# Kernel tuning notes

Measured on AMD Instinct MI355X. Metric: run time of the kernel, lower is better.

The kernel has to match this reference:

```python
import jax, jax.numpy as jnp
import numpy as np
import math

NUM_HEADS = 12
SPARSITY = 0.2


def setup_inputs() -> dict:
    key = jax.random.key(0)
    ks = jax.random.split(key, 4)
    B, N, C = 8, 1024, 768
    x = jax.random.normal(ks[0], (B, N, C), dtype=jnp.float32)
    origin = jax.random.normal(ks[1], (B, N, C), dtype=jnp.float32)
    W_qkv = jax.random.normal(ks[2], (C, 3 * C), dtype=jnp.float32) * (C ** -0.5)
    W_proj = jax.random.normal(ks[3], (C, C), dtype=jnp.float32) * (C ** -0.5)
    b_proj = jnp.zeros((C,), dtype=jnp.float32)
    return {"x": x, "origin": origin, "W_qkv": W_qkv, "W_proj": W_proj, "b_proj": b_proj}


def reference(x, origin, W_qkv, W_proj, b_proj):
    B, N, C = x.shape
    H = NUM_HEADS
    hd = C // H
    scale = hd ** -0.5
    # qkv projection (no bias), split into q,k,v of shape [B,H,N,hd]
    qkv = (x @ W_qkv).reshape(B, N, 3, H, hd).transpose(2, 0, 3, 1, 4)
    q, k, v = qkv[0], qkv[1], qkv[2]
    # scaled scores with constant bias log(1 + N/197); bias is constant so softmax unaffected,
    # but keep it for faithfulness (threshold is taken on post-softmax values anyway)
    logits = jnp.einsum('bhqd,bhkd->bhqk', q * scale, k) + math.log(1.0 + N / 197.0)
    attn = jax.nn.softmax(logits, axis=-1)  # [B,H,N,N]
    # global per-batch threshold: keep top sparsity fraction of all H*N*N scores
    total = H * N * N
    k_idx = int(total * SPARSITY) - 1  # index in descending order
    attn_flat = attn.reshape(B, total)
    thr = jnp.sort(attn_flat, axis=-1)[:, total - 1 - k_idx]  # ascending sort, pick k-th largest
    attn = jnp.where(attn >= thr[:, None, None, None], attn, jnp.zeros((), attn.dtype))
    # attention output, merge heads, project, residual
    out = jnp.einsum('bhqk,bhkd->bhqd', attn, v).transpose(0, 2, 1, 3).reshape(B, N, C)
    out = out @ W_proj + b_proj
    return out + origin
```

## Files before the change

### kernel.cpp

```cpp
#include <hip/hip_runtime.h>
#include <hip/hip_bf16.h>

#define BATCH 8
#define SEQ   1024
#define CDIM  768
#define HEADS 12
#define HD    64

#define NB1    2048
#define TMIN2  (-24.0f)
#define W2     (24.0f / (float)NB1)
#define INV_W2 ((float)NB1 / 24.0f)
#define HLSTR  (NB1 + 8)
#define K_SUB  314573u
#define QSCALE 0.18033688011112042f

typedef __attribute__((ext_vector_type(8)))  short bf16x8;
typedef __attribute__((ext_vector_type(4)))  short bf16x4;
typedef __attribute__((ext_vector_type(4)))  float f32x4;
typedef __attribute__((ext_vector_type(16))) float f32x16;
typedef __attribute__((ext_vector_type(4)))  unsigned u32x4;
typedef __attribute__((ext_vector_type(2)))  unsigned u32x2;

#define MFMA16(a, b, c) __builtin_amdgcn_mfma_f32_16x16x32_bf16(a, b, c, 0, 0, 0)
#define MFMA32(a, b, c) __builtin_amdgcn_mfma_f32_32x32x16_bf16(a, b, c, 0, 0, 0)
#define EXP2(x) __builtin_amdgcn_exp2f(x)
#define LOG2(x) __builtin_amdgcn_logf(x)

__device__ inline unsigned cvtpk(float lo, float hi) {
    unsigned r;
    asm("v_cvt_pk_bf16_f32 %0, %1, %2" : "=v"(r) : "v"(lo), "v"(hi));
    return r;
}

__global__ __launch_bounds__(256) void prep_all(const float* __restrict__ x,
                                                const float* __restrict__ Wq,
                                                const float* __restrict__ Wp,
                                                short* __restrict__ xb,
                                                short* __restrict__ wqt,
                                                short* __restrict__ wpt) {
    __shared__ float ls[64][68];
    int bid = blockIdx.x, tid = threadIdx.x;
    if (bid < 3072) {
        int i = bid * 256 + tid;
        float4 a = *reinterpret_cast<const float4*>(&x[(size_t)i * 8]);
        float4 b = *reinterpret_cast<const float4*>(&x[(size_t)i * 8 + 4]);
        u32x4 w = {cvtpk(a.x, a.y), cvtpk(a.z, a.w), cvtpk(b.x, b.y), cvtpk(b.z, b.w)};
        *reinterpret_cast<u32x4*>(&xb[(size_t)i * 8]) = w;
        return;
    }
    const float* in;
    short* out;
    int C, t;
    if (bid < 3504) { t = bid - 3072; in = Wq; out = wqt; C = 2304; }
    else            { t = bid - 3504; in = Wp; out = wpt; C = 768; }
    int r0 = (t % 12) * 64, c0 = (t / 12) * 64;
#pragma unroll
    for (int it = 0; it < 4; ++it) {
        int rr = it * 16 + (tid >> 4);
        int cc = (tid & 15) * 4;
        float4 d = *reinterpret_cast<const float4*>(&in[(size_t)(r0 + rr) * C + c0 + cc]);
        ls[rr][cc + 0] = d.x; ls[rr][cc + 1] = d.y; ls[rr][cc + 2] = d.z; ls[rr][cc + 3] = d.w;
    }
    __syncthreads();
#pragma unroll
    for (int it = 0; it < 2; ++it) {
        int orow = it * 32 + (tid >> 3);
        int oc = (tid & 7) * 8;
        u32x4 w = {cvtpk(ls[oc + 0][orow], ls[oc + 1][orow]),
                   cvtpk(ls[oc + 2][orow], ls[oc + 3][orow]),
                   cvtpk(ls[oc + 4][orow], ls[oc + 5][orow]),
                   cvtpk(ls[oc + 6][orow], ls[oc + 7][orow])};
        *reinterpret_cast<u32x4*>(&out[(size_t)(c0 + orow) * 768 + r0 + oc]) = w;
    }
}

__global__ __launch_bounds__(256) void qkv_mfma(const short* __restrict__ A,
                                                const short* __restrict__ Bt,
                                                __hip_bfloat16* __restrict__ q,
                                                __hip_bfloat16* __restrict__ k,
                                                __hip_bfloat16* __restrict__ vt) {
    const int K = 768;
    __shared__ short As[128 * 64];
    __shared__ short Bs[128 * 64];
    int tM = blockIdx.x * 128, tN = blockIdx.y * 128;
    int tid = threadIdx.x, wave = tid >> 6, lane = tid & 63, lg = lane >> 4, lc = lane & 15;
    int wr = wave >> 1, wc = wave & 1;
    int srow = tid >> 3, scol = (tid & 7) * 8;
    f32x4 acc[4][4] = {};

    bf16x8 sa[4], sb[4];
#pragma unroll
    for (int j = 0; j < 4; ++j) {
        int r = j * 32 + srow;
        sa[j] = *(const bf16x8*)&A[(size_t)(tM + r) * K + scol];
        sb[j] = *(const bf16x8*)&Bt[(size_t)(tN + r) * K + scol];
    }
#pragma unroll
    for (int j = 0; j < 4; ++j) {
        int r = j * 32 + srow;
        int sw = scol ^ ((r & 7) << 3);
        *(bf16x8*)&As[r * 64 + sw] = sa[j];
        *(bf16x8*)&Bs[r * 64 + sw] = sb[j];
    }
    __syncthreads();

    for (int kc = 0; kc < K; kc += 64) {
        if (kc + 64 < K) {
#pragma unroll
            for (int j = 0; j < 4; ++j) {
                int r = j * 32 + srow;
                sa[j] = *(const bf16x8*)&A[(size_t)(tM + r) * K + kc + 64 + scol];
                sb[j] = *(const bf16x8*)&Bt[(size_t)(tN + r) * K + kc + 64 + scol];
            }
        }
        bf16x8 af[4][2], bfr[4][2];
#pragma unroll
        for (int m4 = 0; m4 < 4; ++m4) {
            int r = wr * 64 + m4 * 16 + lc;
            int sw = (r & 7) << 3;
            af[m4][0] = *(bf16x8*)&As[r * 64 + ((lg * 8) ^ sw)];
            af[m4][1] = *(bf16x8*)&As[r * 64 + ((32 + lg * 8) ^ sw)];
        }
#pragma unroll
        for (int n4 = 0; n4 < 4; ++n4) {
            int r = wc * 64 + n4 * 16 + lc;
            int sw = (r & 7) << 3;
            bfr[n4][0] = *(bf16x8*)&Bs[r * 64 + ((lg * 8) ^ sw)];
            bfr[n4][1] = *(bf16x8*)&Bs[r * 64 + ((32 + lg * 8) ^ sw)];
        }
#pragma unroll
        for (int m4 = 0; m4 < 4; ++m4)
#pragma unroll
            for (int n4 = 0; n4 < 4; ++n4) {
                acc[m4][n4] = MFMA16(af[m4][0], bfr[n4][0], acc[m4][n4]);
                acc[m4][n4] = MFMA16(af[m4][1], bfr[n4][1], acc[m4][n4]);
            }
        __syncthreads();
        if (kc + 64 < K) {
#pragma unroll
            for (int j = 0; j < 4; ++j) {
                int r = j * 32 + srow;
                int sw = scol ^ ((r & 7) << 3);
                *(bf16x8*)&As[r * 64 + sw] = sa[j];
                *(bf16x8*)&Bs[r * 64 + sw] = sb[j];
            }
            __syncthreads();
        }
    }
    int three = tN / 768;
    int cbase = tN - three * 768 + wc * 64;
    if (three == 2) {
#pragma unroll
        for (int m4 = 0; m4 < 4; ++m4) {
            int row0 = tM + wr * 64 + m4 * 16 + lg * 4;
            int b = row0 >> 10, n0 = row0 & 1023;
#pragma unroll
            for (int n4 = 0; n4 < 4; ++n4) {
                int cw = cbase + n4 * 16 + lc;
                int h = cw >> 6, d = cw & 63;
                u32x2 w = {cvtpk(acc[m4][n4][0], acc[m4][n4][1]),
                           cvtpk(acc[m4][n4][2], acc[m4][n4][3])};
                *reinterpret_cast<u32x2*>(
                    &vt[(((size_t)(b * HEADS + h) * 64 + d) << 10) + n0]) = w;
            }
        }
    } else {
        __hip_bfloat16* dst = (three == 0) ? q : k;
#pragma unroll
        for (int m4 = 0; m4 < 4; ++m4)
#pragma unroll
            for (int n4 = 0; n4 < 4; ++n4) {
                int cw = cbase + n4 * 16 + lc;
                int h = cw >> 6, d = cw & 63;
#pragma unroll
                for (int r = 0; r < 4; r += 2) {
                    int row = tM + wr * 64 + m4 * 16 + lg * 4 + r;
                    int b = row >> 10, n = row & 1023;
                    float v0 = acc[m4][n4][r], v1 = acc[m4][n4][r + 1];
                    if (three == 0) { v0 *= QSCALE; v1 *= QSCALE; }
                    unsigned w = cvtpk(v0, v1);
                    size_t base = (((size_t)(b * HEADS + h) << 10) + n) * HD + d;
                    *(unsigned short*)&dst[base] = (unsigned short)w;
                    *(unsigned short*)&dst[base + HD] = (unsigned short)(w >> 16);
                }
            }
    }
}

__global__ __launch_bounds__(256) void stats_mfma(const short* __restrict__ q,
                                                  const short* __restrict__ k,
                                                  float* __restrict__ orow,
                                                  unsigned* __restrict__ hist) {
    __shared__ short kls[8192];
    __shared__ unsigned hl[2 * HLSTR];
    int bid = (blockIdx.x & 7) * 96 + (blockIdx.x >> 3);
    int grp = bid & 7;
    int bh = bid >> 3;
    int b = bh / HEADS;
    int tid = threadIdx.x, wave = tid >> 6, lane = tid & 63;
    int ql = lane & 31, h = lane >> 5;
    const short* kbase = k + (size_t)bh * SEQ * HD;
    int qrow0 = grp * 128 + wave * 32;
    const short* qbase = q + ((size_t)bh * SEQ + qrow0) * HD;
    bf16x8 qf[4];
#pragma unroll
    for (int f = 0; f < 4; ++f)
        qf[f] = *(const bf16x8*)&qbase[ql * 64 + f * 16 + h * 8];

    for (int i = tid; i < 2 * HLSTR; i += 256) hl[i] = 0;

    int srow = tid >> 3, scol = (tid & 7) * 8;
    unsigned scache[4][8];

    bf16x8 st[4];
#pragma unroll
    for (int j = 0; j < 4; ++j)
        st[j] = *(const bf16x8*)&kbase[(size_t)(j * 32 + srow) * 64 + scol];
#pragma unroll
    for (int j = 0; j < 4; ++j) {
        int r = j * 32 + srow;
        *(bf16x8*)&kls[r * 64 + (scol ^ ((r & 7) << 3))] = st[j];
    }
    __syncthreads();
    float lsum = 0.f;
#pragma unroll
    for (int c = 0; c < 8; ++c) {
        if (c < 7) {
#pragma unroll
            for (int j = 0; j < 4; ++j)
                st[j] = *(const bf16x8*)&kbase[(size_t)((c + 1) * 128 + j * 32 + srow) * 64 + scol];
        }
#pragma unroll
        for (int kT = 0; kT < 4; ++kT) {
            f32x16 acc = {};
#pragma unroll
            for (int f = 0; f < 4; ++f) {
                int krow = kT * 32 + ql;
                bf16x8 af = *(bf16x8*)&kls[krow * 64 + ((f * 16 + h * 8) ^ ((krow & 7) << 3))];
                acc = MFMA32(af, qf[f], acc);
            }
            if (kT == 0 && (c & 1) == 0) {
#pragma unroll
                for (int i = 0; i < 8; ++i)
                    scache[c >> 1][i] = cvtpk(acc[2 * i], acc[2 * i + 1]);
            }
            float s = 0.f;
#pragma unroll
            for (int r = 0; r < 16; ++r) s += EXP2(acc[r]);
            lsum += s;
        }
        __syncthreads();
        if (c < 7) {
#pragma unroll
            for (int j = 0; j < 4; ++j) {
                int r = j * 32 + srow;
                *(bf16x8*)&kls[r * 64 + (scol ^ ((r & 7) << 3))] = st[j];
            }
            __syncthreads();
        }
    }
    lsum += __shfl_xor(lsum, 32, 64);
    float o = LOG2(lsum);
    if (h == 0) orow[(size_t)bh * SEQ + qrow0 + ql] = o;

    unsigned coff = (lane & 1) * HLSTR;
#pragma unroll
    for (int cc = 0; cc < 4; ++cc)
#pragma unroll
        for (int i = 0; i < 8; ++i) {
            unsigned w = scache[cc][i];
            float s0 = __builtin_bit_cast(float, w << 16);
            float s1 = __builtin_bit_cast(float, w & 0xffff0000u);
            int b0 = (int)((s0 - o) * INV_W2 + (float)NB1);
            int b1 = (int)((s1 - o) * INV_W2 + (float)NB1);
            b0 = b0 < 0 ? 0 : (b0 > NB1 - 1 ? NB1 - 1 : b0);
            b1 = b1 < 0 ? 0 : (b1 > NB1 - 1 ? NB1 - 1 : b1);
            atomicAdd(&hl[coff + b0], 1u);
            atomicAdd(&hl[coff + b1], 1u);
        }
    __syncthreads();
    unsigned* hb = hist + (size_t)b * NB1;
    for (int i = tid; i < NB1; i += 256) {
        unsigned s = hl[i] + hl[HLSTR + i];
        if (s) atomicAdd(&hb[i], s);
    }
}

__global__ __launch_bounds__(256) void find_thr(const unsigned* __restrict__ hist,
                                                float* __restrict__ thr) {
    __shared__ unsigned cs[256];
    int b = blockIdx.x, tid = threadIdx.x;
    const unsigned* hb = hist + (size_t)b * NB1;
    unsigned s = 0;
#pragma unroll
    for (int i = 0; i < 8; ++i) s += hb[tid * 8 + i];
    cs[tid] = s;
    __syncthreads();
    unsigned suf = 0;
    for (int j = tid; j < 256; ++j) suf += cs[j];
    unsigned above = suf - cs[tid];
    if (suf >= K_SUB && above < K_SUB) {
        unsigned acc = above;
        for (int bb = 7; bb >= 0; --bb) {
            acc += hb[tid * 8 + bb];
            if (acc >= K_SUB) {
                thr[b] = TMIN2 + (float)(tid * 8 + bb) * W2;
                break;
            }
        }
    }
}

__global__ __launch_bounds__(256) void pv_mfma(const short* __restrict__ q,
                                               const short* __restrict__ k,
                                               const short* __restrict__ vt,
                                               const float* __restrict__ orow,
                                               const float* __restrict__ thr,
                                               __hip_bfloat16* __restrict__ aout) {
    __shared__ __align__(16) char smem[32768];
    short* klsA = (short*)smem;
    short* klsB = (short*)(smem + 8192);
    short* vlsA = (short*)(smem + 16384);
    short* vlsB = (short*)(smem + 24576);
    float* comb = (float*)smem;

    int bid = (blockIdx.x & 7) * 192 + (blockIdx.x >> 3);
    int grp = bid & 15;
    int bh = bid >> 4;
    int b = bh / HEADS, hh = bh % HEADS;
    int tid = threadIdx.x, wave = tid >> 6, lane = tid & 63;
    int ql = lane & 31, h = lane >> 5;
    int rh = wave & 1;
    int kh = wave >> 1;
    const short* kbase = k + (size_t)bh * SEQ * HD;
    const short* vtb = vt + (size_t)bh * HD * SEQ;
    int qrow0 = grp * 64 + rh * 32;
    const short* qbase = q + ((size_t)bh * SEQ + qrow0) * HD;
    bf16x8 qf[4];
#pragma unroll
    for (int f = 0; f < 4; ++f)
        qf[f] = *(const bf16x8*)&qbase[ql * 64 + f * 16 + h * 8];
    float o = orow[(size_t)bh * SEQ + qrow0 + ql];
    float tt = thr[b];
    f32x16 oacc[2] = {};
    f32x16 minus_o;
#pragma unroll
    for (int r = 0; r < 16; ++r) minus_o[r] = -o;

    short* kls = kh ? klsB : klsA;
    short* vls = kh ? vlsB : vlsA;

    int sp = tid >> 7;
    int tl = tid & 127;
    int srow = tl >> 3, scol = (tl & 7) * 8;
    short* skls = sp ? klsB : klsA;
    short* svls = sp ? vlsB : vlsA;

    bf16x8 sk[4], sv[4];
    int cc0 = sp * 8;
#pragma unroll
    for (int j = 0; j < 4; ++j) {
        int r = j * 16 + srow;
        sk[j] = *(const bf16x8*)&kbase[(size_t)(cc0 * 64 + r) * 64 + scol];
        sv[j] = *(const bf16x8*)&vtb[((size_t)r << 10) + cc0 * 64 + scol];
    }
#pragma unroll
    for (int j = 0; j < 4; ++j) {
        int r = j * 16 + srow;
        *(bf16x8*)&skls[r * 64 + (scol ^ ((r & 7) << 3))] = sk[j];
        *(bf16x8*)&svls[r * 64 + (scol ^ ((r & 7) << 3))] = sv[j];
    }
    __syncthreads();

    for (int c = 0; c < 8; ++c) {
        if (c < 7) {
            int cc = sp * 8 + c + 1;
#pragma unroll
            for (int j = 0; j < 4; ++j) {
                int r = j * 16 + srow;
                sk[j] = *(const bf16x8*)&kbase[(size_t)(cc * 64 + r) * 64 + scol];
                sv[j] = *(const bf16x8*)&vtb[((size_t)r << 10) + cc * 64 + scol];
            }
        }
#pragma unroll
        for (int kT = 0; kT < 2; ++kT) {
            f32x16 acc = minus_o;
#pragma unroll
            for (int f = 0; f < 4; ++f) {
                int krow = kT * 32 + ql;
                bf16x8 af = *(bf16x8*)&kls[krow * 64 + ((f * 16 + h * 8) ^ ((krow & 7) << 3))];
                acc = MFMA32(af, qf[f], acc);
            }
            float p[16];
#pragma unroll
            for (int r = 0; r < 16; ++r)
                p[r] = (acc[r] >= tt) ? EXP2(acc[r]) : 0.f;
            unsigned c8[8];
#pragma unroll
            for (int i = 0; i < 8; ++i) c8[i] = cvtpk(p[2 * i], p[2 * i + 1]);
#pragma unroll
            for (int s = 0; s < 2; ++s) {
                unsigned a1 = c8[4 * s],     b1 = c8[4 * s + 2];
                unsigned a2 = c8[4 * s + 1], b2 = c8[4 * s + 3];
                asm("v_permlane32_swap_b32 %0, %1" : "+v"(a1), "+v"(b1));
                asm("v_permlane32_swap_b32 %0, %1" : "+v"(a2), "+v"(b2));
                u32x4 W = {a1, a2, b1, b2};
                bf16x8 pa = __builtin_bit_cast(bf16x8, W);
#pragma unroll
                for (int dt = 0; dt < 2; ++dt) {
                    int vrow = dt * 32 + ql;
                    int vcol = (kT * 32 + s * 16 + h * 8) ^ ((vrow & 7) << 3);
                    bf16x8 vf = *(bf16x8*)&vls[vrow * 64 + vcol];
                    oacc[dt] = MFMA32(pa, vf, oacc[dt]);
                }
            }
        }
        __syncthreads();
        if (c < 7) {
#pragma unroll
            for (int j = 0; j < 4; ++j) {
                int r = j * 16 + srow;
                *(bf16x8*)&skls[r * 64 + (scol ^ ((r & 7) << 3))] = sk[j];
                *(bf16x8*)&svls[r * 64 + (scol ^ ((r & 7) << 3))] = sv[j];
            }
            __syncthreads();
        }
    }

    if (kh == 1) {
#pragma unroll
        for (int dt = 0; dt < 2; ++dt)
#pragma unroll
            for (int r = 0; r < 16; ++r) {
                int crow = (r & 3) + 8 * (r >> 2) + 4 * h;
                comb[(rh * 32 + crow) * 65 + dt * 32 + ql] = oacc[dt][r];
            }
    }
    __syncthreads();
    if (kh == 1) return;
#pragma unroll
    for (int dt = 0; dt < 2; ++dt)
#pragma unroll
        for (int r = 0; r < 16; ++r) {
            int crow = (r & 3) + 8 * (r >> 2) + 4 * h;
            oacc[dt][r] += comb[(rh * 32 + crow) * 65 + dt * 32 + ql];
        }
#pragma unroll
    for (int dt = 0; dt < 2; ++dt)
#pragma unroll
        for (int r = 0; r < 16; r += 2) {
            int qr0 = qrow0 + (r & 3) + 8 * (r >> 2) + 4 * h;
            int qr1 = qrow0 + ((r + 1) & 3) + 8 * ((r + 1) >> 2) + 4 * h;
            unsigned w = cvtpk(oacc[dt][r], oacc[dt][r + 1]);
            *(unsigned short*)&aout[((size_t)b * SEQ + qr0) * CDIM + hh * 64 + dt * 32 + ql] =
                (unsigned short)w;
            *(unsigned short*)&aout[((size_t)b * SEQ + qr1) * CDIM + hh * 64 + dt * 32 + ql] =
                (unsigned short)(w >> 16);
        }
}

__global__ __launch_bounds__(256) void proj_mfma(const short* __restrict__ A,
                                                 const short* __restrict__ Bt,
                                                 const float* __restrict__ bias,
                                                 const float* __restrict__ origin,
                                                 float* __restrict__ out) {
    const int K = 768, NN = 768;
    __shared__ short As[128 * 64];
    __shared__ short Bs[128 * 64];
    int tM = blockIdx.x * 128, tN = blockIdx.y * 128;
    int tid = threadIdx.x, wave = tid >> 6, lane = tid & 63, lg = lane >> 4, lc = lane & 15;
    int wr = wave >> 1, wc = wave & 1;
    int srow = tid >> 3, scol = (tid & 7) * 8;
    f32x4 acc[4][4] = {};

    bf16x8 sa[4], sb[4];
#pragma unroll
    for (int j = 0; j < 4; ++j) {
        int r = j * 32 + srow;
        sa[j] = *(const bf16x8*)&A[(size_t)(tM + r) * K + scol];
        sb[j] = *(const bf16x8*)&Bt[(size_t)(tN + r) * K + scol];
    }
#pragma unroll
    for (int j = 0; j < 4; ++j) {
        int r = j * 32 + srow;
        int sw = scol ^ ((r & 7) << 3);
        *(bf16x8*)&As[r * 64 + sw] = sa[j];
        *(bf16x8*)&Bs[r * 64 + sw] = sb[j];
    }
    __syncthreads();

    for (int kc = 0; kc < K; kc += 64) {
        if (kc + 64 < K) {
#pragma unroll
            for (int j = 0; j < 4; ++j) {
                int r = j * 32 + srow;
                sa[j] = *(const bf16x8*)&A[(size_t)(tM + r) * K + kc + 64 + scol];
                sb[j] = *(const bf16x8*)&Bt[(size_t)(tN + r) * K + kc + 64 + scol];
            }
        }
        bf16x8 af[4][2], bfr[4][2];
#pragma unroll
        for (int m4 = 0; m4 < 4; ++m4) {
            int r = wr * 64 + m4 * 16 + lc;
            int sw = (r & 7) << 3;
            af[m4][0] = *(bf16x8*)&As[r * 64 + ((lg * 8) ^ sw)];
            af[m4][1] = *(bf16x8*)&As[r * 64 + ((32 + lg * 8) ^ sw)];
        }
#pragma unroll
        for (int n4 = 0; n4 < 4; ++n4) {
            int r = wc * 64 + n4 * 16 + lc;
            int sw = (r & 7) << 3;
            bfr[n4][0] = *(bf16x8*)&Bs[r * 64 + ((lg * 8) ^ sw)];
            bfr[n4][1] = *(bf16x8*)&Bs[r * 64 + ((32 + lg * 8) ^ sw)];
        }
#pragma unroll
        for (int m4 = 0; m4 < 4; ++m4)
#pragma unroll
            for (int n4 = 0; n4 < 4; ++n4) {
                acc[m4][n4] = MFMA16(af[m4][0], bfr[n4][0], acc[m4][n4]);
                acc[m4][n4] = MFMA16(af[m4][1], bfr[n4][1], acc[m4][n4]);
            }
        __syncthreads();
        if (kc + 64 < K) {
#pragma unroll
            for (int j = 0; j < 4; ++j) {
                int r = j * 32 + srow;
                int sw = scol ^ ((r & 7) << 3);
                *(bf16x8*)&As[r * 64 + sw] = sa[j];
                *(bf16x8*)&Bs[r * 64 + sw] = sb[j];
            }
            __syncthreads();
        }
    }
#pragma unroll
    for (int m4 = 0; m4 < 4; ++m4)
#pragma unroll
        for (int n4 = 0; n4 < 4; ++n4)
#pragma unroll
            for (int r = 0; r < 4; ++r) {
                int row = tM + wr * 64 + m4 * 16 + lg * 4 + r;
                int col = tN + wc * 64 + n4 * 16 + lc;
                out[(size_t)row * NN + col] = acc[m4][n4][r] + bias[col] + origin[(size_t)row * NN + col];
            }
}

extern "C" void kernel_launch(void* const* d_in, const int* in_sizes, int n_in,
                              void* d_out, int out_size, void* d_ws, size_t ws_size,
                              hipStream_t stream) {
    const float* x      = (const float*)d_in[0];
    const float* origin = (const float*)d_in[1];
    const float* W_qkv  = (const float*)d_in[2];
    const float* W_proj = (const float*)d_in[3];
    const float* b_proj = (const float*)d_in[4];
    float* out = (float*)d_out;
    char* ws = (char*)d_ws;

    const size_t QKV_ELEMS = (size_t)BATCH * HEADS * SEQ * HD;
    const size_t X_ELEMS   = (size_t)BATCH * SEQ * CDIM;
    size_t off = 0;
    short* xb  = (short*)(ws + off); off += X_ELEMS * 2;
    short* wqt = (short*)(ws + off); off += (size_t)2304 * 768 * 2;
    short* wpt = (short*)(ws + off); off += (size_t)768 * 768 * 2;
    short* q   = (short*)(ws + off); off += QKV_ELEMS * 2;
    short* k   = (short*)(ws + off); off += QKV_ELEMS * 2;
    short* vt  = (short*)(ws + off); off += QKV_ELEMS * 2;
    short* aoutb = (short*)(ws + off); off += QKV_ELEMS * 2;
    float* orow = (float*)(ws + off); off += (size_t)BATCH * HEADS * SEQ * 4;
    unsigned* hist = (unsigned*)(ws + off); off += (size_t)BATCH * NB1 * 4;
    float* thr = (float*)(ws + off); off += 8 * 4;

    hipMemsetAsync(hist, 0, (size_t)BATCH * NB1 * sizeof(unsigned), stream);
    prep_all<<<dim3(3648), 256, 0, stream>>>(x, W_qkv, W_proj, xb, wqt, wpt);
    qkv_mfma<<<dim3(64, 18), 256, 0, stream>>>(xb, wqt,
                                               (__hip_bfloat16*)q, (__hip_bfloat16*)k, (__hip_bfloat16*)vt);
    stats_mfma<<<dim3(BATCH * HEADS * 8), 256, 0, stream>>>(q, k, orow, hist);
    find_thr<<<dim3(BATCH), 256, 0, stream>>>(hist, thr);
    pv_mfma<<<dim3(BATCH * HEADS * 16), 256, 0, stream>>>(q, k, vt, orow, thr,
                                                          (__hip_bfloat16*)aoutb);
    proj_mfma<<<dim3(64, 6), 256, 0, stream>>>(aoutb, wpt, b_proj, origin, out);
}
```

Before: 158.9 us.

## Fuse x bf16 conversion into QKV GEMM loads and histogram zeroing into prep

```diff
diff --git a/kernel.cpp b/kernel.cpp
--- a/kernel.cpp
+++ b/kernel.cpp
@@ -33,27 +33,19 @@
     return r;
 }
 
-__global__ __launch_bounds__(256) void prep_all(const float* __restrict__ x,
-                                                const float* __restrict__ Wq,
+__global__ __launch_bounds__(256) void prep_all(const float* __restrict__ Wq,
                                                 const float* __restrict__ Wp,
-                                                short* __restrict__ xb,
                                                 short* __restrict__ wqt,
-                                                short* __restrict__ wpt) {
+                                                short* __restrict__ wpt,
+                                                unsigned* __restrict__ hist) {
     __shared__ float ls[64][68];
     int bid = blockIdx.x, tid = threadIdx.x;
-    if (bid < 3072) {
-        int i = bid * 256 + tid;
-        float4 a = *reinterpret_cast<const float4*>(&x[(size_t)i * 8]);
-        float4 b = *reinterpret_cast<const float4*>(&x[(size_t)i * 8 + 4]);
-        u32x4 w = {cvtpk(a.x, a.y), cvtpk(a.z, a.w), cvtpk(b.x, b.y), cvtpk(b.z, b.w)};
-        *reinterpret_cast<u32x4*>(&xb[(size_t)i * 8]) = w;
-        return;
-    }
+    if (bid < 64) hist[bid * 256 + tid] = 0u;
     const float* in;
     short* out;
     int C, t;
-    if (bid < 3504) { t = bid - 3072; in = Wq; out = wqt; C = 2304; }
-    else            { t = bid - 3504; in = Wp; out = wpt; C = 768; }
+    if (bid < 432) { t = bid; in = Wq; out = wqt; C = 2304; }
+    else           { t = bid - 432; in = Wp; out = wpt; C = 768; }
     int r0 = (t % 12) * 64, c0 = (t / 12) * 64;
 #pragma unroll
     for (int it = 0; it < 4; ++it) {
@@ -75,7 +67,7 @@
     }
 }
 
-__global__ __launch_bounds__(256) void qkv_mfma(const short* __restrict__ A,
+__global__ __launch_bounds__(256) void qkv_mfma(const float* __restrict__ X,
                                                 const short* __restrict__ Bt,
                                                 __hip_bfloat16* __restrict__ q,
                                                 __hip_bfloat16* __restrict__ k,
@@ -89,18 +81,21 @@
     int srow = tid >> 3, scol = (tid & 7) * 8;
     f32x4 acc[4][4] = {};
 
-    bf16x8 sa[4], sb[4];
+    u32x4 sa[4];
+    bf16x8 sb[4];
 #pragma unroll
     for (int j = 0; j < 4; ++j) {
         int r = j * 32 + srow;
-        sa[j] = *(const bf16x8*)&A[(size_t)(tM + r) * K + scol];
+        float4 xa = *reinterpret_cast<const float4*>(&X[(size_t)(tM + r) * K + scol]);
+        float4 xb2 = *reinterpret_cast<const float4*>(&X[(size_t)(tM + r) * K + scol + 4]);
+        sa[j] = u32x4{cvtpk(xa.x, xa.y), cvtpk(xa.z, xa.w), cvtpk(xb2.x, xb2.y), cvtpk(xb2.z, xb2.w)};
         sb[j] = *(const bf16x8*)&Bt[(size_t)(tN + r) * K + scol];
     }
 #pragma unroll
     for (int j = 0; j < 4; ++j) {
         int r = j * 32 + srow;
         int sw = scol ^ ((r & 7) << 3);
-        *(bf16x8*)&As[r * 64 + sw] = sa[j];
+        *(u32x4*)&As[r * 64 + sw] = sa[j];
         *(bf16x8*)&Bs[r * 64 + sw] = sb[j];
     }
     __syncthreads();
@@ -110,7 +105,9 @@
 #pragma unroll
             for (int j = 0; j < 4; ++j) {
                 int r = j * 32 + srow;
-                sa[j] = *(const bf16x8*)&A[(size_t)(tM + r) * K + kc + 64 + scol];
+                float4 xa = *reinterpret_cast<const float4*>(&X[(size_t)(tM + r) * K + kc + 64 + scol]);
+                float4 xb2 = *reinterpret_cast<const float4*>(&X[(size_t)(tM + r) * K + kc + 64 + scol + 4]);
+                sa[j] = u32x4{cvtpk(xa.x, xa.y), cvtpk(xa.z, xa.w), cvtpk(xb2.x, xb2.y), cvtpk(xb2.z, xb2.w)};
                 sb[j] = *(const bf16x8*)&Bt[(size_t)(tN + r) * K + kc + 64 + scol];
             }
         }
@@ -142,7 +139,7 @@
             for (int j = 0; j < 4; ++j) {
                 int r = j * 32 + srow;
                 int sw = scol ^ ((r & 7) << 3);
-                *(bf16x8*)&As[r * 64 + sw] = sa[j];
+                *(u32x4*)&As[r * 64 + sw] = sa[j];
                 *(bf16x8*)&Bs[r * 64 + sw] = sb[j];
             }
             __syncthreads();
@@ -557,9 +554,7 @@
     char* ws = (char*)d_ws;
 
     const size_t QKV_ELEMS = (size_t)BATCH * HEADS * SEQ * HD;
-    const size_t X_ELEMS   = (size_t)BATCH * SEQ * CDIM;
     size_t off = 0;
-    short* xb  = (short*)(ws + off); off += X_ELEMS * 2;
     short* wqt = (short*)(ws + off); off += (size_t)2304 * 768 * 2;
     short* wpt = (short*)(ws + off); off += (size_t)768 * 768 * 2;
     short* q   = (short*)(ws + off); off += QKV_ELEMS * 2;
@@ -570,9 +565,8 @@
     unsigned* hist = (unsigned*)(ws + off); off += (size_t)BATCH * NB1 * 4;
     float* thr = (float*)(ws + off); off += 8 * 4;
 
-    hipMemsetAsync(hist, 0, (size_t)BATCH * NB1 * sizeof(unsigned), stream);
-    prep_all<<<dim3(3648), 256, 0, stream>>>(x, W_qkv, W_proj, xb, wqt, wpt);
-    qkv_mfma<<<dim3(64, 18), 256, 0, stream>>>(xb, wqt,
+    prep_all<<<dim3(576), 256, 0, stream>>>(W_qkv, W_proj, wqt, wpt, hist);
+    qkv_mfma<<<dim3(64, 18), 256, 0, stream>>>(x, wqt,
                                                (__hip_bfloat16*)q, (__hip_bfloat16*)k, (__hip_bfloat16*)vt);
     stats_mfma<<<dim3(BATCH * HEADS * 8), 256, 0, stream>>>(q, k, orow, hist);
     find_thr<<<dim3(BATCH), 256, 0, stream>>>(hist, thr);
```

Result: slower. 164.6 us (+3.6%).
